# Optimization experiments

Hardware: AMD Instinct MI355X
Metric: run time of the kernel (lower is better)

The kernel has to match this reference:

```python
import jax, jax.numpy as jnp
import numpy as np

N1, N2 = 4096, 8192
F_M = F_D = 256
OUT, H = 128, 128
CH = 3

def mish(x):
    return x * jnp.tanh(jax.nn.softplus(x))

def setup_inputs() -> dict:
    key = jax.random.key(0)
    ks = jax.random.split(key, 13)
    rn = lambda k, s: jax.random.normal(k, s, dtype=jnp.float32)
    return {
        'm':   rn(ks[0], (N1, F_M)),
        'm1':  rn(ks[1], (N1, F_M)),
        'm2':  rn(ks[2], (N1, F_M)),
        'm_h': rn(ks[3], (N1, H)),
        'd':   rn(ks[4], (N2, F_D)),
        'd1':  rn(ks[5], (N2, F_D)),
        'd2':  rn(ks[6], (N2, F_D)),
        'd_h': rn(ks[7], (N2, H)),
        'w_m': rn(ks[8], (F_M, OUT)) * 0.05,
        'w_d': rn(ks[9], (F_D, OUT)) * 0.05,
        'a_m': rn(ks[10], (1, CH)) * 0.5,
        'a_d': rn(ks[11], (1, CH)) * 0.5,
        'a':   rn(ks[12], (2 * (OUT + H), 1)) * 0.05,
    }

def reference(m, m1, m2, m_h, d, d1, d2, d_h, w_m, w_d, a_m, a_d, a):
    # channel-mix the three views: (1,CH) @ (CH, N*F) -> (N, F)
    m_combine = jnp.concatenate([m, m1, m2], axis=0).reshape(CH, -1)
    h_m = (a_m @ m_combine).reshape(-1, m.shape[1])          # [N1, F_M]
    d_combine = jnp.concatenate([d, d1, d2], axis=0).reshape(CH, -1)
    h_d = (a_d @ d_combine).reshape(-1, d.shape[1])          # [N2, F_D]
    h1qq = jnp.concatenate([h_m @ w_m, m_h], axis=1)         # [N1, OUT+H]
    h2qq = jnp.concatenate([h_d @ w_d, d_h], axis=1)         # [N2, OUT+H]
    # pairwise concat + matmul with `a` == split `a` and outer-sum
    f = h1qq.shape[1]
    a1, a2 = a[:f], a[f:]                                    # each [OUT+H, 1]
    s = mish(h1qq @ a1 + (h2qq @ a2).T)                      # [N1, N2]
    return s
```

## Files before the change

kernel.cpp:

```cpp
#include <hip/hip_runtime.h>

#define N1 4096
#define N2 8192
#define FDIM 256
#define HDIM 128
#define OUTD 128

typedef float fx4 __attribute__((ext_vector_type(4)));

__device__ __forceinline__ float mishf(float x) {
    float e = __expf(fminf(x, 30.0f));
    float w = 1.0f + e;
    float q = __builtin_fmaf(w, w, 1.0f);
    float r = __builtin_amdgcn_rcpf(q);
    return __builtin_fmaf(x, -2.0f * r, x);
}

__global__ void compute_v_kernel(const float* __restrict__ w_m,
                                 const float* __restrict__ w_d,
                                 const float* __restrict__ a,
                                 float* __restrict__ v ) {
    int wave = (blockIdx.x << 2) + (threadIdx.x >> 6);
    int lane = threadIdx.x & 63;
    const float* wr = (wave < 256) ? (w_m + wave * OUTD) : (w_d + (wave - 256) * OUTD);
    const float* av = (wave < 256) ? a : (a + 2 * OUTD);
    float2 wv = ((const float2*)wr)[lane];
    float2 aa = ((const float2*)av)[lane];
    float s = wv.x * aa.x + wv.y * aa.y;
    #pragma unroll
    for (int off = 32; off > 0; off >>= 1) s += __shfl_down(s, off, 64);
    if (lane == 0) v[wave] = s;
}

__global__ void compute_xy_kernel(const float* __restrict__ m,  const float* __restrict__ m1,
                                  const float* __restrict__ m2, const float* __restrict__ m_h,
                                  const float* __restrict__ d,  const float* __restrict__ d1,
                                  const float* __restrict__ d2, const float* __restrict__ d_h,
                                  const float* __restrict__ a_m, const float* __restrict__ a_d,
                                  const float* __restrict__ a,
                                  const float* __restrict__ v,
                                  float* __restrict__ xy ) {
    int gtid = blockIdx.x * blockDim.x + threadIdx.x;
    int row  = gtid >> 6;
    int lane = threadIdx.x & 63;

    const float *pm, *pm1, *pm2, *ph, *pa, *pv;
    float c0, c1, c2;
    int r;
    if (row < N1) {
        r = row;
        pm = m; pm1 = m1; pm2 = m2; ph = m_h;
        pa = a + OUTD;
        pv = v;
        c0 = a_m[0]; c1 = a_m[1]; c2 = a_m[2];
    } else {
        r = row - N1;
        pm = d; pm1 = d1; pm2 = d2; ph = d_h;
        pa = a + 2 * OUTD + HDIM;
        pv = v + 256;
        c0 = a_d[0]; c1 = a_d[1]; c2 = a_d[2];
    }

    fx4 v0 = ((const fx4*)(pm  + (size_t)r * FDIM))[lane];
    fx4 v1 = ((const fx4*)(pm1 + (size_t)r * FDIM))[lane];
    fx4 v2 = ((const fx4*)(pm2 + (size_t)r * FDIM))[lane];
    fx4 vv = ((const fx4*)pv)[lane];

    float val = (c0 * v0.x + c1 * v1.x + c2 * v2.x) * vv.x
              + (c0 * v0.y + c1 * v1.y + c2 * v2.y) * vv.y
              + (c0 * v0.z + c1 * v1.z + c2 * v2.z) * vv.z
              + (c0 * v0.w + c1 * v1.w + c2 * v2.w) * vv.w;

    if (lane < 32) {
        fx4 hv = ((const fx4*)(ph + (size_t)r * HDIM))[lane];
        fx4 av = ((const fx4*)pa)[lane];
        val += hv.x * av.x + hv.y * av.y + hv.z * av.z + hv.w * av.w;
    }

    #pragma unroll
    for (int off = 32; off > 0; off >>= 1) val += __shfl_down(val, off, 64);
    if (lane == 0) xy[row] = val;
}

__global__ void mish_bcast_kernel(const float* __restrict__ x,
                                  const float* __restrict__ y,
                                  fx4* __restrict__ out) {
    const unsigned gtid = blockIdx.x * blockDim.x + threadIdx.x;
    const unsigned wid  = gtid >> 6;
    const unsigned lane = threadIdx.x & 63;
    const unsigned cg   = wid & 15;
    const unsigned rg   = wid >> 4;
    const unsigned c0   = (cg << 7) + lane;
    const fx4* y4 = (const fx4*)y;

    fx4 y0 = y4[c0];
    fx4 y1 = y4[c0 + 64];
    fx4 xa = ((const fx4*)(x + (rg << 3)))[0];
    fx4 xb = ((const fx4*)(x + (rg << 3)))[1];
    float xs[8] = {xa.x, xa.y, xa.z, xa.w, xb.x, xb.y, xb.z, xb.w};

    fx4* o = out + ((size_t)(rg << 3) << 11) + c0;
    #pragma unroll
    for (int rr = 0; rr < 8; ++rr) {
        float xi = xs[rr];
        fx4 r0, r1;
        r0.x = mishf(xi + y0.x);
        r0.y = mishf(xi + y0.y);
        r0.z = mishf(xi + y0.z);
        r0.w = mishf(xi + y0.w);
        r1.x = mishf(xi + y1.x);
        r1.y = mishf(xi + y1.y);
        r1.z = mishf(xi + y1.z);
        r1.w = mishf(xi + y1.w);
        o[0]  = r0;
        o[64] = r1;
        o += 2048;
    }
}

extern "C" void kernel_launch(void* const* d_in, const int* in_sizes, int n_in,
                              void* d_out, int out_size, void* d_ws, size_t ws_size,
                              hipStream_t stream) {
    const float* m   = (const float*)d_in[0];
    const float* m1  = (const float*)d_in[1];
    const float* m2  = (const float*)d_in[2];
    const float* m_h = (const float*)d_in[3];
    const float* d   = (const float*)d_in[4];
    const float* d1  = (const float*)d_in[5];
    const float* d2  = (const float*)d_in[6];
    const float* d_h = (const float*)d_in[7];
    const float* w_m = (const float*)d_in[8];
    const float* w_d = (const float*)d_in[9];
    const float* a_m = (const float*)d_in[10];
    const float* a_d = (const float*)d_in[11];
    const float* a   = (const float*)d_in[12];

    float* wsf = (float*)d_ws;
    float* v  = wsf;
    float* xy = wsf + 512;

    compute_v_kernel<<<128, 256, 0, stream>>>(w_m, w_d, a, v);
    compute_xy_kernel<<<(N1 + N2) / 4, 256, 0, stream>>>(m, m1, m2, m_h, d, d1, d2, d_h,
                                                         a_m, a_d, a, v, xy);
    mish_bcast_kernel<<<2048, 256, 0, stream>>>(xy, xy + N1, (fx4*)d_out);
}
```

Measured before the change: 39.26 us.

## Fuse row-side projection into mish broadcast kernel, one wave per output row

The m-side row reduction (channel mix, projection and m_h dot) moves into the mish broadcast kernel, so each wave computes its own x value and then writes a full output row of 8192 mish values. The y-side projection stays in its own kernel, which now covers only the d rows. This removes the m-side inputs from the separate pass and the x round-trip through workspace. The trade-off is a new per-wave layout: each wave re-reads the whole y vector from cache and loops over the full row, instead of using 8-row tiles that reused y from registers.

```diff
diff --git a/kernel.cpp b/kernel.cpp
--- a/kernel.cpp
+++ b/kernel.cpp
@@ -32,39 +32,21 @@
     if (lane == 0) v[wave] = s;
 }
 
-__global__ void compute_xy_kernel(const float* __restrict__ m,  const float* __restrict__ m1,
-                                  const float* __restrict__ m2, const float* __restrict__ m_h,
-                                  const float* __restrict__ d,  const float* __restrict__ d1,
-                                  const float* __restrict__ d2, const float* __restrict__ d_h,
-                                  const float* __restrict__ a_m, const float* __restrict__ a_d,
-                                  const float* __restrict__ a,
-                                  const float* __restrict__ v,
-                                  float* __restrict__ xy ) {
+__global__ void compute_y_kernel(const float* __restrict__ d,  const float* __restrict__ d1,
+                                 const float* __restrict__ d2, const float* __restrict__ d_h,
+                                 const float* __restrict__ a_d,
+                                 const float* __restrict__ a,
+                                 const float* __restrict__ v,
+                                 float* __restrict__ y ) {
     int gtid = blockIdx.x * blockDim.x + threadIdx.x;
     int row  = gtid >> 6;
     int lane = threadIdx.x & 63;
+    float c0 = a_d[0], c1 = a_d[1], c2 = a_d[2];
 
-    const float *pm, *pm1, *pm2, *ph, *pa, *pv;
-    float c0, c1, c2;
-    int r;
-    if (row < N1) {
-        r = row;
-        pm = m; pm1 = m1; pm2 = m2; ph = m_h;
-        pa = a + OUTD;
-        pv = v;
-        c0 = a_m[0]; c1 = a_m[1]; c2 = a_m[2];
-    } else {
-        r = row - N1;
-        pm = d; pm1 = d1; pm2 = d2; ph = d_h;
-        pa = a + 2 * OUTD + HDIM;
-        pv = v + 256;
-        c0 = a_d[0]; c1 = a_d[1]; c2 = a_d[2];
-    }
-
-    fx4 v0 = ((const fx4*)(pm  + (size_t)r * FDIM))[lane];
-    fx4 v1 = ((const fx4*)(pm1 + (size_t)r * FDIM))[lane];
-    fx4 v2 = ((const fx4*)(pm2 + (size_t)r * FDIM))[lane];
-    fx4 vv = ((const fx4*)pv)[lane];
+    fx4 v0 = ((const fx4*)(d  + (size_t)row * FDIM))[lane];
+    fx4 v1 = ((const fx4*)(d1 + (size_t)row * FDIM))[lane];
+    fx4 v2 = ((const fx4*)(d2 + (size_t)row * FDIM))[lane];
+    fx4 vv = ((const fx4*)(v + 256))[lane];
 
     float val = (c0 * v0.x + c1 * v1.x + c2 * v2.x) * vv.x
               + (c0 * v0.y + c1 * v1.y + c2 * v2.y) * vv.y
@@ -72,49 +54,64 @@
               + (c0 * v0.w + c1 * v1.w + c2 * v2.w) * vv.w;
 
     if (lane < 32) {
-        fx4 hv = ((const fx4*)(ph + (size_t)r * HDIM))[lane];
-        fx4 av = ((const fx4*)pa)[lane];
+        fx4 hv = ((const fx4*)(d_h + (size_t)row * HDIM))[lane];
+        fx4 av = ((const fx4*)(a + 2 * OUTD + HDIM))[lane];
         val += hv.x * av.x + hv.y * av.y + hv.z * av.z + hv.w * av.w;
     }
 
     #pragma unroll
     for (int off = 32; off > 0; off >>= 1) val += __shfl_down(val, off, 64);
-    if (lane == 0) xy[row] = val;
+    if (lane == 0) y[row] = val;
 }
 
-__global__ void mish_bcast_kernel(const float* __restrict__ x,
-                                  const float* __restrict__ y,
-                                  fx4* __restrict__ out) {
-    const unsigned gtid = blockIdx.x * blockDim.x + threadIdx.x;
-    const unsigned wid  = gtid >> 6;
-    const unsigned lane = threadIdx.x & 63;
-    const unsigned cg   = wid & 15;
-    const unsigned rg   = wid >> 4;
-    const unsigned c0   = (cg << 7) + lane;
+__global__ void mish_xbcast_kernel(const float* __restrict__ m,  const float* __restrict__ m1,
+                                   const float* __restrict__ m2, const float* __restrict__ m_h,
+                                   const float* __restrict__ a_m,
+                                   const float* __restrict__ a,
+                                   const float* __restrict__ v,
+                                   const float* __restrict__ y,
+                                   fx4* __restrict__ out) {
+    const int row  = (blockIdx.x << 2) + (threadIdx.x >> 6);
+    const int lane = threadIdx.x & 63;
+    const float c0 = a_m[0], c1 = a_m[1], c2 = a_m[2];
+
+    fx4 v0 = ((const fx4*)(m  + (size_t)row * FDIM))[lane];
+    fx4 v1 = ((const fx4*)(m1 + (size_t)row * FDIM))[lane];
+    fx4 v2 = ((const fx4*)(m2 + (size_t)row * FDIM))[lane];
+    fx4 vv = ((const fx4*)v)[lane];
+
+    float val = (c0 * v0.x + c1 * v1.x + c2 * v2.x) * vv.x
+              + (c0 * v0.y + c1 * v1.y + c2 * v2.y) * vv.y
+              + (c0 * v0.z + c1 * v1.z + c2 * v2.z) * vv.z
+              + (c0 * v0.w + c1 * v1.w + c2 * v2.w) * vv.w;
+
+    if (lane < 32) {
+        fx4 hv = ((const fx4*)(m_h + (size_t)row * HDIM))[lane];
+        fx4 av = ((const fx4*)(a + OUTD))[lane];
+        val += hv.x * av.x + hv.y * av.y + hv.z * av.z + hv.w * av.w;
+    }
+
+    #pragma unroll
+    for (int off = 32; off > 0; off >>= 1) val += __shfl_down(val, off, 64);
+    const float xi = __shfl(val, 0, 64);
+
     const fx4* y4 = (const fx4*)y;
-
-    fx4 y0 = y4[c0];
-    fx4 y1 = y4[c0 + 64];
-    fx4 xa = ((const fx4*)(x + (rg << 3)))[0];
-    fx4 xb = ((const fx4*)(x + (rg << 3)))[1];
-    float xs[8] = {xa.x, xa.y, xa.z, xa.w, xb.x, xb.y, xb.z, xb.w};
-
-    fx4* o = out + ((size_t)(rg << 3) << 11) + c0;
-    #pragma unroll
-    for (int rr = 0; rr < 8; ++rr) {
-        float xi = xs[rr];
+    fx4* o = out + ((size_t)row << 11);
+    #pragma unroll 4
+    for (int c = lane; c < 2048; c += 128) {
+        fx4 ya = y4[c];
+        fx4 yb = y4[c + 64];
         fx4 r0, r1;
-        r0.x = mishf(xi + y0.x);
-        r0.y = mishf(xi + y0.y);
-        r0.z = mishf(xi + y0.z);
-        r0.w = mishf(xi + y0.w);
-        r1.x = mishf(xi + y1.x);
-        r1.y = mishf(xi + y1.y);
-        r1.z = mishf(xi + y1.z);
-        r1.w = mishf(xi + y1.w);
-        o[0]  = r0;
-        o[64] = r1;
-        o += 2048;
+        r0.x = mishf(xi + ya.x);
+        r0.y = mishf(xi + ya.y);
+        r0.z = mishf(xi + ya.z);
+        r0.w = mishf(xi + ya.w);
+        r1.x = mishf(xi + yb.x);
+        r1.y = mishf(xi + yb.y);
+        r1.z = mishf(xi + yb.z);
+        r1.w = mishf(xi + yb.w);
+        o[c]      = r0;
+        o[c + 64] = r1;
     }
 }
 
@@ -136,11 +133,11 @@
     const float* a   = (const float*)d_in[12];
 
     float* wsf = (float*)d_ws;
-    float* v  = wsf;
-    float* xy = wsf + 512;
+    float* v = wsf;
+    float* y = wsf + 512;
 
     compute_v_kernel<<<128, 256, 0, stream>>>(w_m, w_d, a, v);
-    compute_xy_kernel<<<(N1 + N2) / 4, 256, 0, stream>>>(m, m1, m2, m_h, d, d1, d2, d_h,
-                                                         a_m, a_d, a, v, xy);
-    mish_bcast_kernel<<<2048, 256, 0, stream>>>(xy, xy + N1, (fx4*)d_out);
+    compute_y_kernel<<<2048, 256, 0, stream>>>(d, d1, d2, d_h, a_d, a, v, y);
+    mish_xbcast_kernel<<<1024, 256, 0, stream>>>(m, m1, m2, m_h, a_m, a, v, y,
+                                                 (fx4*)d_out);
 }
```

Result: no change. 39.39 us (+0.3%).
